# Performance work log

Hardware: AMD Instinct MI355X
Metric: run time of the kernel (lower is better)

## Reference

```python
import jax, jax.numpy as jnp
import numpy as np

B, S, H, NH = 2, 2048, 1024, 16
HD = H // NH


def setup_inputs() -> dict:
    key = jax.random.key(0)
    ks = jax.random.split(key, 14)
    lim = 1.0 / np.sqrt(H)  # torch Linear default init range
    def lin(ka, kb):
        W = jax.random.uniform(ka, (H, H), jnp.float32, -lim, lim)
        b = jax.random.uniform(kb, (H,), jnp.float32, -lim, lim)
        return W, b
    Wq, bq = lin(ks[0], ks[1])
    Wk, bk = lin(ks[2], ks[3])
    Wv, bv = lin(ks[4], ks[5])
    Wo, bo = lin(ks[6], ks[7])
    return {
        "query": jax.random.normal(ks[8], (B, S, H), jnp.float32),
        "key": jax.random.normal(ks[9], (B, S, H), jnp.float32),
        "value": jax.random.normal(ks[10], (B, S, H), jnp.float32),
        "attn_mask": jax.random.randint(ks[11], (B, S, S), 0, 2).astype(bool),
        "relative_time": jax.random.normal(ks[12], (B, 1, S, S), jnp.float32),
        "Wq": Wq, "bq": bq, "Wk": Wk, "bk": bk,
        "Wv": Wv, "bv": bv, "Wo": Wo, "bo": bo,
    }


def reference(query, key, value, attn_mask, relative_time,
              Wq, bq, Wk, bk, Wv, bv, Wo, bo):
    Bq, Sq, _ = query.shape
    Skv = key.shape[1]
    # projections (torch Linear: x @ W^T + b)
    Q = (query @ Wq.T + bq).reshape(Bq, Sq, NH, HD).transpose(0, 2, 1, 3)
    K = (key @ Wk.T + bk).reshape(Bq, Skv, NH, HD).transpose(0, 2, 1, 3)
    V = (value @ Wv.T + bv).reshape(Bq, Skv, NH, HD).transpose(0, 2, 1, 3)
    scale = HD ** (-0.5)
    # NOTE: bias added BEFORE scaling, matching the original (non-standard)
    scores = jnp.einsum("bhqd,bhkd->bhqk", Q, K)
    scores = (scores + relative_time) * scale
    scores = jnp.where(attn_mask[:, None, :, :], scores, -jnp.inf)
    attn = jax.nn.softmax(scores.astype(jnp.float32), axis=-1).astype(scores.dtype)
    attn = jnp.nan_to_num(attn, nan=0.0)
    # dropout is identity in eval mode (dropout_rate applied only when training)
    out = jnp.einsum("bhqk,bhkd->bhqd", attn, V)
    out = out.transpose(0, 2, 1, 3).reshape(Bq, Sq, H)
    return out @ Wo.T + bo
```

## Files before the change

kernel.cpp:

```cpp
#include <hip/hip_runtime.h>
#include <hip/hip_bf16.h>

constexpr int BATCH = 2, SEQ = 2048, HDIM = 1024, NHEADS = 16, HEADD = 64;
constexpr int MROWS = BATCH * SEQ;
constexpr float QSCALE = 0.18033688011112042f;

typedef short short8  __attribute__((ext_vector_type(8)));
typedef float f32x4   __attribute__((ext_vector_type(4)));
typedef float f32x16  __attribute__((ext_vector_type(16)));
typedef int   int4v   __attribute__((ext_vector_type(4)));
typedef unsigned short ushort4v __attribute__((ext_vector_type(4)));

static __device__ __forceinline__ short f2bf(float f) {
    __hip_bfloat16 h = __float2bfloat16(f);
    return *reinterpret_cast<short*>(&h);
}

static __device__ __forceinline__ int cvt_pk_bf16(float a, float b) {
    int r;
    asm("v_cvt_pk_bf16_f32 %0, %1, %2" : "=v"(r) : "v"(a), "v"(b));
    return r;
}

static __device__ __forceinline__ float bfbits2f(unsigned short u) {
    return __builtin_bit_cast(float, (unsigned int)u << 16);
}

static __device__ __forceinline__ void gload_lds16(const void* g, void* l) {
    __builtin_amdgcn_global_load_lds(
        (const __attribute__((address_space(1))) unsigned int*)g,
        (__attribute__((address_space(3))) unsigned int*)l, 16, 0, 0);
}

static __device__ __forceinline__ int swz(int row) {
    return (((row & 7) ^ ((row >> 3) & 3))) << 4;
}

__global__ void cvt_all_kernel(const float* __restrict__ q, const float* __restrict__ k,
                               const float* __restrict__ v, const float* __restrict__ w0,
                               const float* __restrict__ w1, const float* __restrict__ w2,
                               const float* __restrict__ w3,
                               short* __restrict__ xq, short* __restrict__ xk,
                               short* __restrict__ xv, short* __restrict__ o0,
                               short* __restrict__ o1, short* __restrict__ o2,
                               short* __restrict__ o3, int n4x, int n4w) {
    int i = blockIdx.x * blockDim.x + threadIdx.x;
    const int stride = gridDim.x * blockDim.x;
    const int total = 3 * n4x + 4 * n4w;
    for (; i < total; i += stride) {
        const float* in; short* out; int j = i;
        if (j < 3 * n4x) {
            if (j >= 2 * n4x)      { in = v; out = xv; j -= 2 * n4x; }
            else if (j >= n4x)     { in = k; out = xk; j -= n4x; }
            else                   { in = q; out = xq; }
        } else {
            j -= 3 * n4x;
            if (j >= 3 * n4w)      { in = w3; out = o3; j -= 3 * n4w; }
            else if (j >= 2 * n4w) { in = w2; out = o2; j -= 2 * n4w; }
            else if (j >= n4w)     { in = w1; out = o1; j -= n4w; }
            else                   { in = w0; out = o0; }
        }
        const float4 val = reinterpret_cast<const float4*>(in)[j];
        short4 o;
        o.x = f2bf(val.x); o.y = f2bf(val.y); o.z = f2bf(val.z); o.w = f2bf(val.w);
        reinterpret_cast<short4*>(out)[j] = o;
    }
}

__global__ void detect_mask_kernel(const unsigned int* __restrict__ m, int* flag) {
    const int tid = threadIdx.x;
    int gt1 = 0, isf = 0;
    for (int i = 0; i < 4; ++i) {
        unsigned int wv = m[tid + 256 * i];
        if (wv > 1u) gt1 = 1;
        if (wv == 0x3F800000u) isf = 1;
    }
    __shared__ int s_gt1, s_isf;
    if (tid == 0) { s_gt1 = 0; s_isf = 0; }
    __syncthreads();
    if (gt1) atomicOr(&s_gt1, 1);
    if (isf) atomicOr(&s_isf, 1);
    __syncthreads();
    if (tid == 0) flag[0] = s_gt1 ? (s_isf ? 2 : 1) : 0;
}

__global__ void fuse_rel_kernel(const float* __restrict__ rel, const void* __restrict__ mask,
                                const int* __restrict__ flag, short* __restrict__ rT,
                                int nThr) {
    const int f = flag[0];
    int i = blockIdx.x * blockDim.x + threadIdx.x;
    const int stride = gridDim.x * blockDim.x;
    for (; i < nThr; i += stride) {
        const int q    = i & 2047;
        const int kv16 = (i >> 11) & 127;
        const int b    = i >> 18;
        const long base = ((long)(b * 2048 + q)) * 2048 + kv16 * 16;
        float4 rv[4];
        #pragma unroll
        for (int g = 0; g < 4; ++g)
            rv[g] = *reinterpret_cast<const float4*>(rel + base + 4 * g);
        bool mk[16];
        if (f == 1) {
            const unsigned int* mp = (const unsigned int*)((const unsigned char*)mask + base);
            #pragma unroll
            for (int wd = 0; wd < 4; ++wd) {
                const unsigned int mw = mp[wd];
                #pragma unroll
                for (int s = 0; s < 4; ++s) mk[wd * 4 + s] = ((mw >> (8 * s)) & 0xffu) != 0;
            }
        } else if (f == 0) {
            const int* mp = (const int*)mask + base;
            #pragma unroll
            for (int j = 0; j < 16; ++j) mk[j] = mp[j] != 0;
        } else {
            const float* mp = (const float*)mask + base;
            #pragma unroll
            for (int j = 0; j < 16; ++j) mk[j] = mp[j] != 0.0f;
        }
        const float* rp = reinterpret_cast<const float*>(&rv[0]);
        #pragma unroll
        for (int g = 0; g < 4; ++g) {
            short4 o;
            short* op = reinterpret_cast<short*>(&o);
            #pragma unroll
            for (int j = 0; j < 4; ++j) {
                const int idx = 4 * g + j;
                op[j] = f2bf(mk[idx] ? rp[idx] * QSCALE : -1e30f);
            }
            *reinterpret_cast<short4*>(rT + (((long)(b * 512 + kv16 * 4 + g)) * 2048 + q) * 4) = o;
        }
    }
}

template<int BN, typename EPI>
static __device__ __forceinline__
void gemm_core(const short* A, const short* Bw, int K, int m0, int n0, EPI epi) {
    constexpr int NFRAG = BN / 32;
    __shared__ short As[128 * 64];
    __shared__ short Bs[BN * 64];
    const int tid  = threadIdx.x;
    const int lane = tid & 63;
    const int w    = tid >> 6;
    const int lo   = lane & 15, hi = lane >> 4;
    const int wm   = w >> 1, wn = w & 1;

    f32x4 acc[4][NFRAG] = {};

    const int arow  = tid >> 3;
    const int acolb = (tid & 7) * 16;
    const int scolS = acolb ^ swz(arow);
    const char* Ab = (const char*)A + ((long)(m0 + arow) * K) * 2 + scolS;
    const char* Bb = (const char*)Bw + ((long)(n0 + arow) * K) * 2 + scolS;

    for (int k0 = 0; k0 < K; k0 += 64) {
        #pragma unroll
        for (int i = 0; i < 4; ++i)
            gload_lds16(Ab + ((long)i * 32 * K + k0) * 2, (char*)As + i * 4096 + tid * 16);
        #pragma unroll
        for (int i = 0; i < NFRAG; ++i)
            gload_lds16(Bb + ((long)i * 32 * K + k0) * 2, (char*)Bs + i * 4096 + tid * 16);
        __syncthreads();
        #pragma unroll
        for (int ks = 0; ks < 2; ++ks) {
            short8 af[4], bf[NFRAG];
            #pragma unroll
            for (int fm = 0; fm < 4; ++fm) {
                const int row = wm * 64 + fm * 16 + lo;
                af[fm] = *reinterpret_cast<const short8*>(
                    (const char*)As + row * 128 + ((ks * 64 + hi * 16) ^ swz(row)));
            }
            #pragma unroll
            for (int fn = 0; fn < NFRAG; ++fn) {
                const int row = wn * (BN / 2) + fn * 16 + lo;
                bf[fn] = *reinterpret_cast<const short8*>(
                    (const char*)Bs + row * 128 + ((ks * 64 + hi * 16) ^ swz(row)));
            }
            #pragma unroll
            for (int fm = 0; fm < 4; ++fm)
                #pragma unroll
                for (int fn = 0; fn < NFRAG; ++fn)
                    acc[fm][fn] = __builtin_amdgcn_mfma_f32_16x16x32_bf16(
                        af[fm], bf[fn], acc[fm][fn], 0, 0, 0);
        }
        __syncthreads();
    }

    #pragma unroll
    for (int fm = 0; fm < 4; ++fm)
        #pragma unroll
        for (int fn = 0; fn < NFRAG; ++fn) {
            const int n = n0 + wn * (BN / 2) + fn * 16 + lo;
            const int mB = m0 + wm * 64 + fm * 16 + hi * 4;
            for (int r = 0; r < 4; ++r) epi(mB + r, n, acc[fm][fn][r]);
        }
}

__global__ __launch_bounds__(256, 3)
void qkv_gemm(const short* xq, const short* xk, const short* xv,
              const short* wq, const short* wk, const short* wv,
              const float* bq, const float* bk, const float* bv,
              short* Qb, short* Kb, short* Vt) {
    const int which = blockIdx.x >> 8;
    const int bid   = blockIdx.x & 255;
    const int m0 = (bid >> 3) << 7;
    const int n0 = (bid & 7) << 7;
    const short* A    = which == 0 ? xq : which == 1 ? xk : xv;
    const short* W    = which == 0 ? wq : which == 1 ? wk : wv;
    const float* bias = which == 0 ? bq : which == 1 ? bk : bv;
    short* C          = which == 0 ? Qb : which == 1 ? Kb : Vt;
    const float scale = which == 0 ? QSCALE : 1.0f;
    gemm_core<128>(A, W, HDIM, m0, n0, [&](int m, int n, float v) {
        v = (v + bias[n]) * scale;
        const int b = m >> 11, s = m & (SEQ - 1);
        const int h = n >> 6, d = n & 63;
        long idx;
        if (which != 2) idx = (((long)(b * NHEADS + h)) * SEQ + s) * HEADD + d;
        else            idx = (((long)(b * NHEADS + h)) * HEADD + d) * SEQ + s;
        C[idx] = f2bf(v);
    });
}

__global__ __launch_bounds__(256, 2)
void out_gemm(const short* A, const short* W, const float* bias, float* Cout) {
    const int bid = blockIdx.x;
    const int m0 = (bid >> 4) << 7;
    const int n0 = (bid & 15) << 6;
    gemm_core<64>(A, W, HDIM, m0, n0, [&](int m, int n, float v) {
        Cout[(long)m * HDIM + n] = v + bias[n];
    });
}

__global__ __launch_bounds__(256, 4)
void attn_fwd(const short* __restrict__ Qb, const short* __restrict__ Kb,
              const short* __restrict__ Vtb, const short* __restrict__ rT,
              short* __restrict__ Ob) {
    __shared__ short Ks[2][64 * 64];
    __shared__ short Vs[2][64 * 64];
    const int tid  = threadIdx.x;
    const int lane = tid & 63;
    const int wv   = tid >> 6;
    const int qp   = wv & 1;
    const int t    = wv >> 1;
    const int l31  = lane & 31, hi2 = lane >> 5;
    const int wg = ((blockIdx.x & 7) << 7) + (blockIdx.x >> 3);
    const int qt = wg & 31, h = (wg >> 5) & 15, b = wg >> 9;
    const int bh = b * NHEADS + h;
    const int q0 = qt * 64 + qp * 32 + l31;

    short8 qf[4];
    {
        const short* qp_ = Qb + ((long)bh * SEQ + q0) * HEADD + hi2 * 8;
        #pragma unroll
        for (int s = 0; s < 4; ++s)
            qf[s] = *reinterpret_cast<const short8*>(qp_ + s * 16);
    }

    float lsum = 0.0f;
    f32x16 oacc0 = {}, oacc1 = {};

    const int srow  = tid >> 3;
    const int scolb = (tid & 7) * 16;
    const int scolK = scolb ^ swz(srow);
    const char* KbB = (const char*)Kb + ((long)bh * SEQ + srow) * 128 + scolK;
    const char* VbB = (const char*)Vtb + ((long)bh * HEADD + srow) * ((long)SEQ * 2) + scolK;

    auto stage = [&](int buf, int kt) {
        #pragma unroll
        for (int i = 0; i < 2; ++i) {
            gload_lds16(KbB + ((long)kt * 64 + i * 32) * 128,
                        (char*)&Ks[buf][0] + i * 4096 + tid * 16);
            gload_lds16(VbB + (long)i * 32 * (SEQ * 2) + (long)kt * 128,
                        (char*)&Vs[buf][0] + i * 4096 + tid * 16);
        }
    };

    ushort4v rbuf[4];
    auto loadRel = [&](int kt) {
        #pragma unroll
        for (int g = 0; g < 4; ++g) {
            const int p4 = kt * 16 + t * 8 + 2 * g + hi2;
            rbuf[g] = *reinterpret_cast<const ushort4v*>(
                rT + (((long)(b * 512 + p4)) * 2048 + q0) * 4);
        }
    };

    stage(0, 0);
    loadRel(0);

    const int rsw = swz(l31);
    const int NT = SEQ / 64;

    for (int kt = 0; kt < NT; ++kt) {
        const int cb = kt & 1;
        const bool hasNext = (kt < NT - 1);
        if (hasNext) stage(cb ^ 1, kt + 1);
        if (hasNext) asm volatile("s_waitcnt vmcnt(4)" ::: "memory");
        else         asm volatile("s_waitcnt vmcnt(0)" ::: "memory");
        __builtin_amdgcn_s_barrier();
        asm volatile("" ::: "memory");

        f32x16 sc;
        #pragma unroll
        for (int g = 0; g < 4; ++g)
            #pragma unroll
            for (int j = 0; j < 4; ++j)
                sc[4 * g + j] = bfbits2f(rbuf[g][j]);
        if (hasNext) loadRel(kt + 1);

        const char* kls = (const char*)&Ks[cb][0];
        const char* kr  = kls + (t * 32 + l31) * 128;
        __builtin_amdgcn_s_setprio(1);
        #pragma unroll
        for (int s = 0; s < 4; ++s) {
            short8 kf = *reinterpret_cast<const short8*>(kr + ((s * 32 + hi2 * 16) ^ rsw));
            sc = __builtin_amdgcn_mfma_f32_32x32x16_bf16(kf, qf[s], sc, 0, 0, 0);
        }
        __builtin_amdgcn_s_setprio(0);

        int X[8];
        #pragma unroll
        for (int i2 = 0; i2 < 8; ++i2) {
            const float p0 = __builtin_amdgcn_exp2f(sc[2 * i2]);
            const float p1 = __builtin_amdgcn_exp2f(sc[2 * i2 + 1]);
            lsum += p0 + p1;
            X[i2] = cvt_pk_bf16(p0, p1);
        }
        int pa[2][4];
        #pragma unroll
        for (int u = 0; u < 2; ++u) {
            auto r0 = __builtin_amdgcn_permlane32_swap(X[4 * u + 0], X[4 * u + 2], false, false);
            auto r1 = __builtin_amdgcn_permlane32_swap(X[4 * u + 1], X[4 * u + 3], false, false);
            pa[u][0] = (int)r0[0];
            pa[u][1] = (int)r1[0];
            pa[u][2] = (int)r0[1];
            pa[u][3] = (int)r1[1];
        }

        const char* vls = (const char*)&Vs[cb][0];
        __builtin_amdgcn_s_setprio(1);
        #pragma unroll
        for (int dt = 0; dt < 2; ++dt) {
            const char* vr = vls + (dt * 32 + l31) * 128;
            #pragma unroll
            for (int u = 0; u < 2; ++u) {
                const int s = 2 * t + u;
                short8 vf = *reinterpret_cast<const short8*>(vr + ((s * 32 + hi2 * 16) ^ rsw));
                int4v pw = { pa[u][0], pa[u][1], pa[u][2], pa[u][3] };
                if (dt == 0)
                    oacc0 = __builtin_amdgcn_mfma_f32_32x32x16_bf16(
                        __builtin_bit_cast(short8, pw), vf, oacc0, 0, 0, 0);
                else
                    oacc1 = __builtin_amdgcn_mfma_f32_32x32x16_bf16(
                        __builtin_bit_cast(short8, pw), vf, oacc1, 0, 0, 0);
            }
        }
        __builtin_amdgcn_s_setprio(0);

        asm volatile("" ::: "memory");
        __builtin_amdgcn_s_barrier();
    }

    lsum += __shfl_xor(lsum, 32, 64);

    float* cmbO = (float*)&Ks[0][0];
    float* cmbL = (float*)&Vs[0][0];
    if (t == 1) {
        #pragma unroll
        for (int r = 0; r < 16; ++r) {
            const int qloc = (r & 3) + 8 * (r >> 2) + 4 * hi2;
            cmbO[(qp * 32 + qloc) * 64 + l31]      = oacc0[r];
            cmbO[(qp * 32 + qloc) * 64 + 32 + l31] = oacc1[r];
        }
        if (hi2 == 0) cmbL[qp * 32 + l31] = lsum;
    }
    __syncthreads();
    if (t == 0) {
        const float ltot = lsum + cmbL[qp * 32 + l31];
        const float inv  = ltot > 0.0f ? 1.0f / ltot : 0.0f;
        #pragma unroll
        for (int r = 0; r < 16; ++r) {
            const int qloc = (r & 3) + 8 * (r >> 2) + 4 * hi2;
            const float invr = __shfl(inv, qloc, 64);
            const int qg = qt * 64 + qp * 32 + qloc;
            const long obase = ((long)b * SEQ + qg) * HDIM + h * 64 + l31;
            const float o0 = oacc0[r] + cmbO[(qp * 32 + qloc) * 64 + l31];
            const float o1 = oacc1[r] + cmbO[(qp * 32 + qloc) * 64 + 32 + l31];
            Ob[obase]      = f2bf(o0 * invr);
            Ob[obase + 32] = f2bf(o1 * invr);
        }
    }
}

extern "C" void kernel_launch(void* const* d_in, const int* in_sizes, int n_in,
                              void* d_out, int out_size, void* d_ws, size_t ws_size,
                              hipStream_t stream) {
    const float* q    = (const float*)d_in[0];
    const float* k    = (const float*)d_in[1];
    const float* v    = (const float*)d_in[2];
    const void*  mask = d_in[3];
    const float* rel  = (const float*)d_in[4];
    const float* Wq   = (const float*)d_in[5];
    const float* bq   = (const float*)d_in[6];
    const float* Wk   = (const float*)d_in[7];
    const float* bk   = (const float*)d_in[8];
    const float* Wv   = (const float*)d_in[9];
    const float* bv   = (const float*)d_in[10];
    const float* Wo   = (const float*)d_in[11];
    const float* bo   = (const float*)d_in[12];
    (void)in_sizes; (void)n_in; (void)out_size; (void)ws_size;

    char* ws = (char*)d_ws;
    size_t off = 0;
    auto alloc = [&](size_t bytes) {
        char* p = ws + off;
        off += (bytes + 255) & ~(size_t)255;
        return p;
    };
    const size_t xBytes = (size_t)MROWS * HDIM * 2;
    const size_t wBytes = (size_t)HDIM * HDIM * 2;
    const size_t poolBytes = 3 * xBytes + 3 * wBytes;

    short* Qb  = (short*)alloc(xBytes);
    short* Kb  = (short*)alloc(xBytes);
    short* Vt  = (short*)alloc(xBytes);
    short* wob = (short*)alloc(wBytes);
    int*   flag = (int*)alloc(256);
    char* pool = (char*)alloc(poolBytes);
    short* Ab  = (short*)alloc(xBytes);

    short* xq  = (short*)(pool);
    short* xk  = (short*)(pool + xBytes);
    short* xv  = (short*)(pool + 2 * xBytes);
    short* wqb = (short*)(pool + 3 * xBytes);
    short* wkb = (short*)(pool + 3 * xBytes + wBytes);
    short* wvb = (short*)(pool + 3 * xBytes + 2 * wBytes);
    short* rT  = (short*)(pool);

    const int n4x = MROWS * HDIM / 4, n4w = HDIM * HDIM / 4;
    cvt_all_kernel<<<2048, 256, 0, stream>>>(q, k, v, Wq, Wk, Wv, Wo,
                                             xq, xk, xv, wqb, wkb, wvb, wob, n4x, n4w);
    detect_mask_kernel<<<1, 256, 0, stream>>>((const unsigned int*)mask, flag);

    qkv_gemm<<<768, 256, 0, stream>>>(xq, xk, xv, wqb, wkb, wvb,
                                      bq, bk, bv, Qb, Kb, Vt);

    const int relThr = BATCH * 128 * 2048;
    fuse_rel_kernel<<<2048, 256, 0, stream>>>(rel, mask, flag, rT, relThr);

    attn_fwd<<<1024, 256, 0, stream>>>(Qb, Kb, Vt, rT, Ab);

    out_gemm<<<512, 256, 0, stream>>>(Ab, wob, bo, (float*)d_out);
}
```

Baseline: 157.9 us.

## Triple-buffer GEMM LDS loads and move attention barrier to one per tile

Replaces the single-buffered GEMM core with a 3-stage LDS ring that keeps two k-tiles of loads in flight and needs one barrier per step. The QKV GEMM switches to 128x64 tiles with twice as many blocks. In the attention kernel the next tile is now staged after a single barrier at the top of each iteration, dropping the trailing barrier but waiting on all loads (vmcnt(0)). This trades more LDS per block and lower occupancy for better hiding of memory latency, and the attention change may expose more load latency.

```diff
diff --git a/kernel.cpp b/kernel.cpp
--- a/kernel.cpp
+++ b/kernel.cpp
@@ -132,19 +132,18 @@
     }
 }
 
-template<int BN, typename EPI>
+template<typename EPI>
 static __device__ __forceinline__
-void gemm_core(const short* A, const short* Bw, int K, int m0, int n0, EPI epi) {
-    constexpr int NFRAG = BN / 32;
-    __shared__ short As[128 * 64];
-    __shared__ short Bs[BN * 64];
+void gemm_core64(const short* A, const short* Bw, int K, int m0, int n0, EPI epi) {
+    __shared__ short As[3][128 * 64];
+    __shared__ short Bs[3][64 * 64];
     const int tid  = threadIdx.x;
     const int lane = tid & 63;
     const int w    = tid >> 6;
     const int lo   = lane & 15, hi = lane >> 4;
     const int wm   = w >> 1, wn = w & 1;
 
-    f32x4 acc[4][NFRAG] = {};
+    f32x4 acc[4][2] = {};
 
     const int arow  = tid >> 3;
     const int acolb = (tid & 7) * 16;
@@ -152,64 +151,76 @@
     const char* Ab = (const char*)A + ((long)(m0 + arow) * K) * 2 + scolS;
     const char* Bb = (const char*)Bw + ((long)(n0 + arow) * K) * 2 + scolS;
 
-    for (int k0 = 0; k0 < K; k0 += 64) {
+    auto stage = [&](int buf, int k0) {
         #pragma unroll
         for (int i = 0; i < 4; ++i)
-            gload_lds16(Ab + ((long)i * 32 * K + k0) * 2, (char*)As + i * 4096 + tid * 16);
-        #pragma unroll
-        for (int i = 0; i < NFRAG; ++i)
-            gload_lds16(Bb + ((long)i * 32 * K + k0) * 2, (char*)Bs + i * 4096 + tid * 16);
-        __syncthreads();
+            gload_lds16(Ab + ((long)i * 32 * K + k0) * 2, (char*)&As[buf][0] + i * 4096 + tid * 16);
+        #pragma unroll
+        for (int i = 0; i < 2; ++i)
+            gload_lds16(Bb + ((long)i * 32 * K + k0) * 2, (char*)&Bs[buf][0] + i * 4096 + tid * 16);
+    };
+
+    const int nsteps = K >> 6;
+    stage(0, 0);
+    stage(1, 64);
+
+    for (int j = 0; j < nsteps; ++j) {
+        const int buf = j % 3;
+        if (j == nsteps - 1) asm volatile("s_waitcnt vmcnt(0)" ::: "memory");
+        else                 asm volatile("s_waitcnt vmcnt(6)" ::: "memory");
+        __builtin_amdgcn_s_barrier();
+        asm volatile("" ::: "memory");
+        if (j + 2 < nsteps) stage((j + 2) % 3, (j + 2) * 64);
+
         #pragma unroll
         for (int ks = 0; ks < 2; ++ks) {
-            short8 af[4], bf[NFRAG];
+            short8 af[4], bf[2];
             #pragma unroll
             for (int fm = 0; fm < 4; ++fm) {
                 const int row = wm * 64 + fm * 16 + lo;
                 af[fm] = *reinterpret_cast<const short8*>(
-                    (const char*)As + row * 128 + ((ks * 64 + hi * 16) ^ swz(row)));
+                    (const char*)&As[buf][0] + row * 128 + ((ks * 64 + hi * 16) ^ swz(row)));
             }
             #pragma unroll
-            for (int fn = 0; fn < NFRAG; ++fn) {
-                const int row = wn * (BN / 2) + fn * 16 + lo;
+            for (int fn = 0; fn < 2; ++fn) {
+                const int row = wn * 32 + fn * 16 + lo;
                 bf[fn] = *reinterpret_cast<const short8*>(
-                    (const char*)Bs + row * 128 + ((ks * 64 + hi * 16) ^ swz(row)));
+                    (const char*)&Bs[buf][0] + row * 128 + ((ks * 64 + hi * 16) ^ swz(row)));
             }
             #pragma unroll
             for (int fm = 0; fm < 4; ++fm)
                 #pragma unroll
-                for (int fn = 0; fn < NFRAG; ++fn)
+                for (int fn = 0; fn < 2; ++fn)
                     acc[fm][fn] = __builtin_amdgcn_mfma_f32_16x16x32_bf16(
                         af[fm], bf[fn], acc[fm][fn], 0, 0, 0);
         }
-        __syncthreads();
     }
 
     #pragma unroll
     for (int fm = 0; fm < 4; ++fm)
         #pragma unroll
-        for (int fn = 0; fn < NFRAG; ++fn) {
-            const int n = n0 + wn * (BN / 2) + fn * 16 + lo;
+        for (int fn = 0; fn < 2; ++fn) {
+            const int n = n0 + wn * 32 + fn * 16 + lo;
             const int mB = m0 + wm * 64 + fm * 16 + hi * 4;
             for (int r = 0; r < 4; ++r) epi(mB + r, n, acc[fm][fn][r]);
         }
 }
 
-__global__ __launch_bounds__(256, 3)
+__global__ __launch_bounds__(256, 2)
 void qkv_gemm(const short* xq, const short* xk, const short* xv,
               const short* wq, const short* wk, const short* wv,
               const float* bq, const float* bk, const float* bv,
               short* Qb, short* Kb, short* Vt) {
-    const int which = blockIdx.x >> 8;
-    const int bid   = blockIdx.x & 255;
-    const int m0 = (bid >> 3) << 7;
-    const int n0 = (bid & 7) << 7;
+    const int which = blockIdx.x >> 9;
+    const int bid   = blockIdx.x & 511;
+    const int m0 = (bid >> 4) << 7;
+    const int n0 = (bid & 15) << 6;
     const short* A    = which == 0 ? xq : which == 1 ? xk : xv;
     const short* W    = which == 0 ? wq : which == 1 ? wk : wv;
     const float* bias = which == 0 ? bq : which == 1 ? bk : bv;
     short* C          = which == 0 ? Qb : which == 1 ? Kb : Vt;
     const float scale = which == 0 ? QSCALE : 1.0f;
-    gemm_core<128>(A, W, HDIM, m0, n0, [&](int m, int n, float v) {
+    gemm_core64(A, W, HDIM, m0, n0, [&](int m, int n, float v) {
         v = (v + bias[n]) * scale;
         const int b = m >> 11, s = m & (SEQ - 1);
         const int h = n >> 6, d = n & 63;
@@ -225,7 +236,7 @@
     const int bid = blockIdx.x;
     const int m0 = (bid >> 4) << 7;
     const int n0 = (bid & 15) << 6;
-    gemm_core<64>(A, W, HDIM, m0, n0, [&](int m, int n, float v) {
+    gemm_core64(A, W, HDIM, m0, n0, [&](int m, int n, float v) {
         Cout[(long)m * HDIM + n] = v + bias[n];
     });
 }
@@ -292,12 +303,10 @@
 
     for (int kt = 0; kt < NT; ++kt) {
         const int cb = kt & 1;
-        const bool hasNext = (kt < NT - 1);
-        if (hasNext) stage(cb ^ 1, kt + 1);
-        if (hasNext) asm volatile("s_waitcnt vmcnt(4)" ::: "memory");
-        else         asm volatile("s_waitcnt vmcnt(0)" ::: "memory");
+        asm volatile("s_waitcnt vmcnt(0)" ::: "memory");
         __builtin_amdgcn_s_barrier();
         asm volatile("" ::: "memory");
+        if (kt + 1 < NT) stage(cb ^ 1, kt + 1);
 
         f32x16 sc;
         #pragma unroll
@@ -305,7 +314,7 @@
             #pragma unroll
             for (int j = 0; j < 4; ++j)
                 sc[4 * g + j] = bfbits2f(rbuf[g][j]);
-        if (hasNext) loadRel(kt + 1);
+        if (kt + 1 < NT) loadRel(kt + 1);
 
         const char* kls = (const char*)&Ks[cb][0];
         const char* kr  = kls + (t * 32 + l31) * 128;
@@ -355,12 +364,11 @@
             }
         }
         __builtin_amdgcn_s_setprio(0);
-
-        asm volatile("" ::: "memory");
-        __builtin_amdgcn_s_barrier();
     }
 
     lsum += __shfl_xor(lsum, 32, 64);
+
+    __syncthreads();
 
     float* cmbO = (float*)&Ks[0][0];
     float* cmbL = (float*)&Vs[0][0];
@@ -441,8 +449,8 @@
                                              xq, xk, xv, wqb, wkb, wvb, wob, n4x, n4w);
     detect_mask_kernel<<<1, 256, 0, stream>>>((const unsigned int*)mask, flag);
 
-    qkv_gemm<<<768, 256, 0, stream>>>(xq, xk, xv, wqb, wkb, wvb,
-                                      bq, bk, bv, Qb, Kb, Vt);
+    qkv_gemm<<<1536, 256, 0, stream>>>(xq, xk, xv, wqb, wkb, wvb,
+                                       bq, bk, bv, Qb, Kb, Vt);
 
     const int relThr = BATCH * 128 * 2048;
     fuse_rel_kernel<<<2048, 256, 0, stream>>>(rel, mask, flag, rT, relThr);
```

Measured after the change: 161.8 us. 1.02x slower.

## Single-barrier K/V pipeline and two-ahead relative-time prefetch in attention loop

Applied to the files above, without the earlier changes.

Restructures the attention main loop so each iteration uses one barrier. The barrier comes first, then the next K/V tile is staged, which removes the trailing barrier per tile. The relative-time bias is now double-buffered two tiles ahead in two register sets, and the loop is manually unrolled by two so buffer selection is static. This aims to hide global load latency and cut synchronisation. In exchange it raises register pressure, and the vmcnt accounting now has to cover both the extra in-flight loads and the new ordering.

```diff
diff --git a/kernel.cpp b/kernel.cpp
--- a/kernel.cpp
+++ b/kernel.cpp
@@ -274,93 +274,98 @@
         }
     };
 
-    ushort4v rbuf[4];
-    auto loadRel = [&](int kt) {
+    ushort4v rbA[4], rbB[4];
+    const short* rTb = rT + ((long)b * 512 * 2048 + (long)q0) * 4;
+    auto loadRel = [&](ushort4v* rb, int kt) {
         #pragma unroll
         for (int g = 0; g < 4; ++g) {
             const int p4 = kt * 16 + t * 8 + 2 * g + hi2;
-            rbuf[g] = *reinterpret_cast<const ushort4v*>(
-                rT + (((long)(b * 512 + p4)) * 2048 + q0) * 4);
+            rb[g] = *reinterpret_cast<const ushort4v*>(rTb + (long)p4 * 2048 * 4);
         }
     };
 
     stage(0, 0);
-    loadRel(0);
+    loadRel(rbA, 0);
+    loadRel(rbB, 1);
 
     const int rsw = swz(l31);
     const int NT = SEQ / 64;
 
-    for (int kt = 0; kt < NT; ++kt) {
-        const int cb = kt & 1;
-        const bool hasNext = (kt < NT - 1);
-        if (hasNext) stage(cb ^ 1, kt + 1);
-        if (hasNext) asm volatile("s_waitcnt vmcnt(4)" ::: "memory");
-        else         asm volatile("s_waitcnt vmcnt(0)" ::: "memory");
-        __builtin_amdgcn_s_barrier();
-        asm volatile("" ::: "memory");
-
-        f32x16 sc;
-        #pragma unroll
-        for (int g = 0; g < 4; ++g)
-            #pragma unroll
-            for (int j = 0; j < 4; ++j)
-                sc[4 * g + j] = bfbits2f(rbuf[g][j]);
-        if (hasNext) loadRel(kt + 1);
-
-        const char* kls = (const char*)&Ks[cb][0];
-        const char* kr  = kls + (t * 32 + l31) * 128;
-        __builtin_amdgcn_s_setprio(1);
-        #pragma unroll
-        for (int s = 0; s < 4; ++s) {
-            short8 kf = *reinterpret_cast<const short8*>(kr + ((s * 32 + hi2 * 16) ^ rsw));
-            sc = __builtin_amdgcn_mfma_f32_32x32x16_bf16(kf, qf[s], sc, 0, 0, 0);
-        }
-        __builtin_amdgcn_s_setprio(0);
-
-        int X[8];
-        #pragma unroll
-        for (int i2 = 0; i2 < 8; ++i2) {
-            const float p0 = __builtin_amdgcn_exp2f(sc[2 * i2]);
-            const float p1 = __builtin_amdgcn_exp2f(sc[2 * i2 + 1]);
-            lsum += p0 + p1;
-            X[i2] = cvt_pk_bf16(p0, p1);
-        }
-        int pa[2][4];
-        #pragma unroll
-        for (int u = 0; u < 2; ++u) {
-            auto r0 = __builtin_amdgcn_permlane32_swap(X[4 * u + 0], X[4 * u + 2], false, false);
-            auto r1 = __builtin_amdgcn_permlane32_swap(X[4 * u + 1], X[4 * u + 3], false, false);
-            pa[u][0] = (int)r0[0];
-            pa[u][1] = (int)r1[0];
-            pa[u][2] = (int)r0[1];
-            pa[u][3] = (int)r1[1];
-        }
-
-        const char* vls = (const char*)&Vs[cb][0];
-        __builtin_amdgcn_s_setprio(1);
-        #pragma unroll
-        for (int dt = 0; dt < 2; ++dt) {
-            const char* vr = vls + (dt * 32 + l31) * 128;
+    #pragma unroll 1
+    for (int kt = 0; kt < NT; kt += 2) {
+        #pragma unroll
+        for (int half = 0; half < 2; ++half) {
+            const int ki = kt + half;
+            const int cb = ki & 1;
+            const ushort4v* rb = half == 0 ? rbA : rbB;
+            const bool tailWait = (ki + 2 >= NT) && (half == 1);
+            if (tailWait) asm volatile("s_waitcnt vmcnt(0)" ::: "memory");
+            else          asm volatile("s_waitcnt vmcnt(4)" ::: "memory");
+            __builtin_amdgcn_s_barrier();
+            asm volatile("" ::: "memory");
+            if (ki + 1 < NT) stage(cb ^ 1, ki + 1);
+
+            f32x16 sc;
+            #pragma unroll
+            for (int g = 0; g < 4; ++g)
+                #pragma unroll
+                for (int j = 0; j < 4; ++j)
+                    sc[4 * g + j] = bfbits2f(rb[g][j]);
+            if (ki + 2 < NT) loadRel(half == 0 ? rbA : rbB, ki + 2);
+
+            const char* kr = (const char*)&Ks[cb][0] + (t * 32 + l31) * 128;
+            __builtin_amdgcn_s_setprio(1);
+            #pragma unroll
+            for (int s = 0; s < 4; ++s) {
+                short8 kf = *reinterpret_cast<const short8*>(kr + ((s * 32 + hi2 * 16) ^ rsw));
+                sc = __builtin_amdgcn_mfma_f32_32x32x16_bf16(kf, qf[s], sc, 0, 0, 0);
+            }
+            __builtin_amdgcn_s_setprio(0);
+
+            int X[8];
+            #pragma unroll
+            for (int i2 = 0; i2 < 8; ++i2) {
+                const float p0 = __builtin_amdgcn_exp2f(sc[2 * i2]);
+                const float p1 = __builtin_amdgcn_exp2f(sc[2 * i2 + 1]);
+                lsum += p0 + p1;
+                X[i2] = cvt_pk_bf16(p0, p1);
+            }
+            int pa[2][4];
             #pragma unroll
             for (int u = 0; u < 2; ++u) {
-                const int s = 2 * t + u;
-                short8 vf = *reinterpret_cast<const short8*>(vr + ((s * 32 + hi2 * 16) ^ rsw));
-                int4v pw = { pa[u][0], pa[u][1], pa[u][2], pa[u][3] };
-                if (dt == 0)
-                    oacc0 = __builtin_amdgcn_mfma_f32_32x32x16_bf16(
-                        __builtin_bit_cast(short8, pw), vf, oacc0, 0, 0, 0);
-                else
-                    oacc1 = __builtin_amdgcn_mfma_f32_32x32x16_bf16(
-                        __builtin_bit_cast(short8, pw), vf, oacc1, 0, 0, 0);
-            }
-        }
-        __builtin_amdgcn_s_setprio(0);
-
-        asm volatile("" ::: "memory");
-        __builtin_amdgcn_s_barrier();
+                auto r0 = __builtin_amdgcn_permlane32_swap(X[4 * u + 0], X[4 * u + 2], false, false);
+                auto r1 = __builtin_amdgcn_permlane32_swap(X[4 * u + 1], X[4 * u + 3], false, false);
+                pa[u][0] = (int)r0[0];
+                pa[u][1] = (int)r1[0];
+                pa[u][2] = (int)r0[1];
+                pa[u][3] = (int)r1[1];
+            }
+
+            const char* vls = (const char*)&Vs[cb][0];
+            __builtin_amdgcn_s_setprio(1);
+            #pragma unroll
+            for (int dt = 0; dt < 2; ++dt) {
+                const char* vr = vls + (dt * 32 + l31) * 128;
+                #pragma unroll
+                for (int u = 0; u < 2; ++u) {
+                    const int s = 2 * t + u;
+                    short8 vf = *reinterpret_cast<const short8*>(vr + ((s * 32 + hi2 * 16) ^ rsw));
+                    int4v pw = { pa[u][0], pa[u][1], pa[u][2], pa[u][3] };
+                    if (dt == 0)
+                        oacc0 = __builtin_amdgcn_mfma_f32_32x32x16_bf16(
+                            __builtin_bit_cast(short8, pw), vf, oacc0, 0, 0, 0);
+                    else
+                        oacc1 = __builtin_amdgcn_mfma_f32_32x32x16_bf16(
+                            __builtin_bit_cast(short8, pw), vf, oacc1, 0, 0, 0);
+                }
+            }
+            __builtin_amdgcn_s_setprio(0);
+        }
     }
 
     lsum += __shfl_xor(lsum, 32, 64);
+
+    __syncthreads();
 
     float* cmbO = (float*)&Ks[0][0];
     float* cmbL = (float*)&Vs[0][0];
```

Result: slower. 170.2 us (+7.8%).
